# Optimization experiments

Measured on AMD Instinct MI355X. Metric: run time of the kernel, lower is better.

The kernel has to match this reference:

```python
import jax, jax.numpy as jnp
import numpy as np

N_HEAD, D_MODEL, D_K, D_V = 16, 1024, 64, 64
LN_EPS = 1e-5


def setup_inputs() -> dict:
    key = jax.random.key(0)
    ks = jax.random.split(key, 10)
    B, S = 2, 2048
    s = 1.0 / np.sqrt(D_MODEL)
    return {
        "q": jax.random.normal(ks[0], (B, S, D_MODEL), jnp.float32),
        "k": jax.random.normal(ks[1], (B, S, D_MODEL), jnp.float32),
        "v": jax.random.normal(ks[2], (B, S, D_MODEL), jnp.float32),
        "w_q": jax.random.normal(ks[3], (D_MODEL, N_HEAD * D_K), jnp.float32) * s,
        "w_k": jax.random.normal(ks[4], (D_MODEL, N_HEAD * D_K), jnp.float32) * s,
        "w_v": jax.random.normal(ks[5], (D_MODEL, N_HEAD * D_V), jnp.float32) * s,
        "w_fc": jax.random.normal(ks[6], (N_HEAD * D_V, D_MODEL), jnp.float32) * s,
        "b_fc": jnp.zeros((D_MODEL,), jnp.float32),
        "ln_g": jnp.ones((D_MODEL,), jnp.float32),
        "ln_b": jnp.zeros((D_MODEL,), jnp.float32),
    }


def _mha(q, k, v, w_q, w_k, w_v, w_fc, b_fc, ln_g, ln_b):
    B, S, _ = q.shape
    residual = q
    # projections -> [B, H, S, Dh]
    qh = (q @ w_q).reshape(B, S, N_HEAD, D_K).transpose(0, 2, 1, 3)
    kh = (k @ w_k).reshape(B, S, N_HEAD, D_K).transpose(0, 2, 1, 3)
    vh = (v @ w_v).reshape(B, S, N_HEAD, D_V).transpose(0, 2, 1, 3)
    # NOTE: original scales by sqrt(d_model), not sqrt(d_k)
    temper = jnp.sqrt(jnp.asarray(D_MODEL, qh.dtype))
    attn = jnp.einsum("bhqd,bhkd->bhqk", qh, kh) / temper
    attn = jax.nn.softmax(attn, axis=-1)  # dropout = identity (eval mode)
    out = jnp.einsum("bhqk,bhkd->bhqd", attn, vh)
    out = out.transpose(0, 2, 1, 3).reshape(B, S, N_HEAD * D_V)
    out = out @ w_fc + b_fc  # dropout = identity (eval mode)
    x = out + residual
    mu = jnp.mean(x, axis=-1, keepdims=True)
    var = jnp.var(x, axis=-1, keepdims=True)
    x = (x - mu) * jax.lax.rsqrt(var + LN_EPS) * ln_g + ln_b
    return x, attn


def reference(q, k, v, w_q, w_k, w_v, w_fc, b_fc, ln_g, ln_b):
    return _mha(q, k, v, w_q, w_k, w_v, w_fc, b_fc, ln_g, ln_b)
```

## Files before the change

kernel.cpp:

```cpp
#include <hip/hip_runtime.h>
#include <hip/hip_bf16.h>
#include <stdint.h>

typedef __attribute__((ext_vector_type(8))) short bf16x8;
typedef __attribute__((ext_vector_type(4))) float f32x4;

#define GLOAD16(gptr, lptr)                                              \
  __builtin_amdgcn_global_load_lds(                                      \
      (const __attribute__((address_space(1))) void*)(gptr),             \
      (__attribute__((address_space(3))) void*)(lptr), 16, 0, 0)

__device__ __forceinline__ uint32_t pack_bf16_2(float a, float b) {
  union { __hip_bfloat16 h; unsigned short u; } ca, cb;
  ca.h = __float2bfloat16(a); cb.h = __float2bfloat16(b);
  return (uint32_t)ca.u | ((uint32_t)cb.u << 16);
}

__global__ __launch_bounds__(256)
void prep_kernel(const float* __restrict__ q, const float* __restrict__ k,
                 const float* __restrict__ v,
                 __hip_bfloat16* __restrict__ q_bf, __hip_bfloat16* __restrict__ k_bf,
                 __hip_bfloat16* __restrict__ v_bf,
                 const float* __restrict__ w0, const float* __restrict__ w1,
                 const float* __restrict__ w2, const float* __restrict__ w3,
                 __hip_bfloat16* __restrict__ o0, __hip_bfloat16* __restrict__ o1,
                 __hip_bfloat16* __restrict__ o2, __hip_bfloat16* __restrict__ o3)
{
  const int blk = blockIdx.x;
  if (blk < 6144) {
    const int z = blk >> 11;
    const int bx = blk & 2047;
    const float* in = z == 0 ? q : z == 1 ? k : v;
    __hip_bfloat16* out = z == 0 ? q_bf : z == 1 ? k_bf : v_bf;
    long i = ((long)bx * 256 + threadIdx.x) * 8;
    float4 a = *(const float4*)(in + i);
    float4 b = *(const float4*)(in + i + 4);
    uint4 r;
    r.x = pack_bf16_2(a.x, a.y); r.y = pack_bf16_2(a.z, a.w);
    r.z = pack_bf16_2(b.x, b.y); r.w = pack_bf16_2(b.z, b.w);
    *(uint4*)(out + i) = r;
  } else {
    __shared__ float t[64][65];
    const int w = blk - 6144;
    const int z = w >> 8;
    const int by = (w >> 4) & 15, bx = w & 15;
    const float* in = z == 0 ? w0 : z == 1 ? w1 : z == 2 ? w2 : w3;
    __hip_bfloat16* out = z == 0 ? o0 : z == 1 ? o1 : z == 2 ? o2 : o3;
    const int tx = threadIdx.x & 15, ty = threadIdx.x >> 4;
    for (int i = 0; i < 4; ++i)
      for (int j = 0; j < 4; ++j)
        t[ty*4+i][tx*4+j] = in[(long)(by*64 + ty*4+i)*1024 + bx*64 + tx*4 + j];
    __syncthreads();
    for (int i = 0; i < 4; ++i)
      for (int j = 0; j < 4; ++j)
        out[(long)(bx*64 + ty*4+i)*1024 + by*64 + tx*4 + j] =
            __float2bfloat16(t[tx*4+j][ty*4+i]);
  }
}

__global__ __launch_bounds__(256)
void vtrans_kernel(const __hip_bfloat16* __restrict__ in, __hip_bfloat16* __restrict__ out)
{
  __shared__ __hip_bfloat16 t[64][72];
  const int tx = threadIdx.x & 15, ty = threadIdx.x >> 4;
  const int sb = blockIdx.x, bh = blockIdx.y;
  const __hip_bfloat16* inp = in + (long)bh * 2048 * 64;
  __hip_bfloat16* outp = out + (long)bh * 64 * 2048;
  for (int i = 0; i < 4; ++i)
    for (int j = 0; j < 4; ++j)
      t[ty*4+i][tx*4+j] = inp[(long)(sb*64 + ty*4+i)*64 + tx*4 + j];
  __syncthreads();
  for (int i = 0; i < 4; ++i)
    for (int j = 0; j < 4; ++j)
      outp[(long)(ty*4+i)*2048 + sb*64 + tx*4 + j] = t[tx*4+j][ty*4+i];
}

template<int EPI>
__global__ __launch_bounds__(256)
void gemm_bt(const __hip_bfloat16* __restrict__ A0,
             const __hip_bfloat16* __restrict__ A1,
             const __hip_bfloat16* __restrict__ A2,
             const __hip_bfloat16* __restrict__ B0,
             const __hip_bfloat16* __restrict__ B1,
             const __hip_bfloat16* __restrict__ B2,
             void* __restrict__ out,
             const float* __restrict__ bias,
             const float* __restrict__ resid,
             int M, int N, int K)
{
  const int z = (EPI == 0) ? blockIdx.z : 0;
  const __hip_bfloat16* A  = z == 0 ? A0 : z == 1 ? A1 : A2;
  const __hip_bfloat16* Bt = z == 0 ? B0 : z == 1 ? B1 : B2;
  const float scale = (EPI == 0 && z == 0) ? 0.045084219f : 1.0f;

  __shared__ __hip_bfloat16 As[128*32];
  __shared__ __hip_bfloat16 Bs[128*32];
  const int tid = threadIdx.x;
  const int wid = tid >> 6;
  const int lane = tid & 63;
  const int lr = lane & 15, lg = lane >> 4;
  const int bm = blockIdx.y, bn = blockIdx.x;
  const int wm = wid >> 1, wn = wid & 1;

  f32x4 acc[4][4] = {};

  const int srow = tid >> 2;
  const int scol = (tid & 3) * 8;
  const __hip_bfloat16* Ag = A  + (long)(bm*128 + srow)*K + scol;
  const __hip_bfloat16* Bg = Bt + (long)(bn*128 + srow)*K + scol;
  __hip_bfloat16* AsW = &As[wid*512];
  __hip_bfloat16* BsW = &Bs[wid*512];

  for (int k0 = 0; k0 < K; k0 += 32) {
    GLOAD16(Ag + k0,          AsW);
    GLOAD16(Ag + 64*K + k0,   AsW + 2048);
    GLOAD16(Bg + k0,          BsW);
    GLOAD16(Bg + 64*K + k0,   BsW + 2048);
    __syncthreads();
    bf16x8 a[4], b[4];
    for (int m = 0; m < 4; ++m)
      a[m] = *(const bf16x8*)&As[(wm*64 + m*16 + lr)*32 + lg*8];
    for (int n = 0; n < 4; ++n)
      b[n] = *(const bf16x8*)&Bs[(wn*64 + n*16 + lr)*32 + lg*8];
    for (int m = 0; m < 4; ++m)
      for (int n = 0; n < 4; ++n)
        acc[m][n] = __builtin_amdgcn_mfma_f32_16x16x32_bf16(b[n], a[m], acc[m][n], 0, 0, 0);
    __syncthreads();
  }

  for (int m = 0; m < 4; ++m) {
    const int grow = bm*128 + wm*64 + m*16 + lr;
    for (int n = 0; n < 4; ++n) {
      const int c0 = bn*128 + wn*64 + n*16 + lg*4;
      if (EPI == 0) {
        const int b_ = grow >> 11, s = grow & 2047;
        const int h = c0 >> 6, d = c0 & 63;
        uint2 pk;
        pk.x = pack_bf16_2(acc[m][n][0]*scale, acc[m][n][1]*scale);
        pk.y = pack_bf16_2(acc[m][n][2]*scale, acc[m][n][3]*scale);
        *(uint2*)((__hip_bfloat16*)out + (long)z*4194304 +
                  ((long)(b_*16 + h)*2048 + s)*64 + d) = pk;
      } else {
        float4 b4 = *(const float4*)(bias + c0);
        float4 r4 = *(const float4*)(resid + (long)grow*N + c0);
        float4 o4;
        o4.x = acc[m][n][0] + b4.x + r4.x;
        o4.y = acc[m][n][1] + b4.y + r4.y;
        o4.z = acc[m][n][2] + b4.z + r4.z;
        o4.w = acc[m][n][3] + b4.w + r4.w;
        *(float4*)((float*)out + (long)grow*N + c0) = o4;
      }
    }
  }
}

__global__ __launch_bounds__(256, 4)
void attn_kernel(const __hip_bfloat16* __restrict__ Qh,
                 const __hip_bfloat16* __restrict__ Kh,
                 const __hip_bfloat16* __restrict__ Vt,
                 float* __restrict__ attn_out,
                 __hip_bfloat16* __restrict__ O)
{
  __shared__ __hip_bfloat16 Ps[64*128];
  __shared__ float red[4][64];
  __shared__ float invl[64];

  const int tid = threadIdx.x, wid = tid >> 6, lane = tid & 63;
  const int lr = lane & 15, lg = lane >> 4;
  const int orig = (blockIdx.x & 7) * 128 + (blockIdx.x >> 3);
  const int bh = orig >> 5, qb = orig & 31;

  const __hip_bfloat16* Qlane = Qh + ((long)bh*2048 + qb*64 + lr)*64 + lg*8;
  const __hip_bfloat16* Klane = Kh + (long)bh*2048*64 + (long)(wid*32 + lr)*64 + lg*8;
  const __hip_bfloat16* Vlane = Vt + (long)bh*64*2048 + (long)(wid*16 + lr)*2048 + lg*8;

  bf16x8 aq[4][2];
  for (int mq = 0; mq < 4; ++mq)
    for (int kk = 0; kk < 2; ++kk)
      aq[mq][kk] = *(const bf16x8*)(Qlane + mq*1024 + kk*32);

  float rs[4] = {0.f, 0.f, 0.f, 0.f};
  for (int kt = 0; kt < 16; ++kt) {
    bf16x8 bk[2][2];
    for (int nk = 0; nk < 2; ++nk)
      for (int kk = 0; kk < 2; ++kk)
        bk[nk][kk] = *(const bf16x8*)(Klane + kt*8192 + nk*1024 + kk*32);
    f32x4 s2[4][2] = {};
    for (int mq = 0; mq < 4; ++mq)
      for (int nk = 0; nk < 2; ++nk)
        for (int kk = 0; kk < 2; ++kk)
          s2[mq][nk] = __builtin_amdgcn_mfma_f32_16x16x32_bf16(bk[nk][kk], aq[mq][kk], s2[mq][nk], 0, 0, 0);
    for (int mq = 0; mq < 4; ++mq)
      for (int nk = 0; nk < 2; ++nk)
        for (int jj = 0; jj < 4; ++jj)
          rs[mq] += exp2f(s2[mq][nk][jj]);
  }

  for (int mq = 0; mq < 4; ++mq) {
    float e = rs[mq];
    e += __shfl_xor(e, 16);
    e += __shfl_xor(e, 32);
    rs[mq] = e;
  }
  if (lg == 0)
    for (int mq = 0; mq < 4; ++mq)
      red[wid][mq*16 + lr] = rs[mq];
  __syncthreads();
  if (tid < 64)
    invl[tid] = 1.0f / (red[0][tid] + red[1][tid] + red[2][tid] + red[3][tid]);
  __syncthreads();

  float iv[4];
  for (int mq = 0; mq < 4; ++mq) iv[mq] = invl[mq*16 + lr];

  f32x4 acc_o[4] = {};
  float* attn_row = attn_out + ((long)bh*2048 + qb*64)*2048;

#pragma unroll 1
  for (int kt = 0; kt < 16; ++kt) {
    bf16x8 bk[2][2], vb[4];
#pragma unroll
    for (int nk = 0; nk < 2; ++nk)
      for (int kk = 0; kk < 2; ++kk)
        bk[nk][kk] = *(const bf16x8*)(Klane + kt*8192 + nk*1024 + kk*32);
#pragma unroll
    for (int k2 = 0; k2 < 4; ++k2)
      vb[k2] = *(const bf16x8*)(Vlane + kt*128 + k2*32);

    f32x4 s2[4][2] = {};
    __builtin_amdgcn_s_setprio(1);
#pragma unroll
    for (int mq = 0; mq < 4; ++mq)
      for (int nk = 0; nk < 2; ++nk)
        for (int kk = 0; kk < 2; ++kk)
          s2[mq][nk] = __builtin_amdgcn_mfma_f32_16x16x32_bf16(bk[nk][kk], aq[mq][kk], s2[mq][nk], 0, 0, 0);
    __builtin_amdgcn_s_setprio(0);

#pragma unroll
    for (int mq = 0; mq < 4; ++mq) {
      const int row = mq*16 + lr;
      for (int nk = 0; nk < 2; ++nk) {
        const int kc = wid*32 + nk*16 + lg*4;
        f32x4 p;
        p[0] = exp2f(s2[mq][nk][0]) * iv[mq];
        p[1] = exp2f(s2[mq][nk][1]) * iv[mq];
        p[2] = exp2f(s2[mq][nk][2]) * iv[mq];
        p[3] = exp2f(s2[mq][nk][3]) * iv[mq];
        __builtin_nontemporal_store(p, (f32x4*)(attn_row + (long)row*2048 + kt*128 + kc));
        uint2 pb;
        pb.x = pack_bf16_2(p[0], p[1]);
        pb.y = pack_bf16_2(p[2], p[3]);
        const int boff = (row*256 + kc*2) ^ ((row & 15) << 4);
        *(uint2*)((char*)Ps + boff) = pb;
      }
    }
    __syncthreads();

    __builtin_amdgcn_s_setprio(1);
#pragma unroll
    for (int mq = 0; mq < 4; ++mq) {
      const int row = mq*16 + lr;
      for (int k2 = 0; k2 < 4; ++k2) {
        const int boff = (row*256 + (k2*32 + lg*8)*2) ^ ((row & 15) << 4);
        bf16x8 pa = *(const bf16x8*)((char*)Ps + boff);
        acc_o[mq] = __builtin_amdgcn_mfma_f32_16x16x32_bf16(vb[k2], pa, acc_o[mq], 0, 0, 0);
      }
    }
    __builtin_amdgcn_s_setprio(0);
    __syncthreads();
  }

  const int b_ = bh >> 4, h = bh & 15;
  for (int mq = 0; mq < 4; ++mq) {
    const long grow = (long)b_*2048 + qb*64 + mq*16 + lr;
    const int col = h*64 + wid*16 + lg*4;
    uint2 pk;
    pk.x = pack_bf16_2(acc_o[mq][0], acc_o[mq][1]);
    pk.y = pack_bf16_2(acc_o[mq][2], acc_o[mq][3]);
    *(uint2*)(O + grow*1024 + col) = pk;
  }
}

__global__ __launch_bounds__(256)
void ln_kernel(const float* __restrict__ xin, const float* __restrict__ gam,
               const float* __restrict__ bet, float* __restrict__ xout)
{
  const int row = blockIdx.x;
  const int tid = threadIdx.x;
  const float* xr = xin + (long)row*1024;
  float4 v = *(const float4*)(xr + tid*4);
  float s  = v.x + v.y + v.z + v.w;
  float ss = v.x*v.x + v.y*v.y + v.z*v.z + v.w*v.w;
  for (int o = 1; o < 64; o <<= 1) {
    s  += __shfl_xor(s, o, 64);
    ss += __shfl_xor(ss, o, 64);
  }
  __shared__ float rsh[4], rssh[4];
  const int wid = tid >> 6, lane = tid & 63;
  if (lane == 0) { rsh[wid] = s; rssh[wid] = ss; }
  __syncthreads();
  s  = rsh[0] + rsh[1] + rsh[2] + rsh[3];
  ss = rssh[0] + rssh[1] + rssh[2] + rssh[3];
  const float mean = s * (1.0f/1024.0f);
  const float var  = ss * (1.0f/1024.0f) - mean*mean;
  const float rstd = rsqrtf(var + 1e-5f);
  float4 g4 = *(const float4*)(gam + tid*4);
  float4 b4 = *(const float4*)(bet + tid*4);
  float4 o4;
  o4.x = (v.x - mean)*rstd*g4.x + b4.x;
  o4.y = (v.y - mean)*rstd*g4.y + b4.y;
  o4.z = (v.z - mean)*rstd*g4.z + b4.z;
  o4.w = (v.w - mean)*rstd*g4.w + b4.w;
  *(float4*)(xout + (long)row*1024 + tid*4) = o4;
}

extern "C" void kernel_launch(void* const* d_in, const int* in_sizes, int n_in,
                              void* d_out, int out_size, void* d_ws, size_t ws_size,
                              hipStream_t stream)
{
  (void)in_sizes; (void)n_in; (void)out_size; (void)ws_size;
  const float* q    = (const float*)d_in[0];
  const float* k    = (const float*)d_in[1];
  const float* v    = (const float*)d_in[2];
  const float* w_q  = (const float*)d_in[3];
  const float* w_k  = (const float*)d_in[4];
  const float* w_v  = (const float*)d_in[5];
  const float* w_fc = (const float*)d_in[6];
  const float* b_fc = (const float*)d_in[7];
  const float* ln_g = (const float*)d_in[8];
  const float* ln_b = (const float*)d_in[9];

  const long MB = 1024*1024;
  char* ws = (char*)d_ws;
  __hip_bfloat16* q_bf  = (__hip_bfloat16*)(ws);
  __hip_bfloat16* k_bf  = (__hip_bfloat16*)(ws +  8*MB);
  __hip_bfloat16* v_bf  = (__hip_bfloat16*)(ws + 16*MB);
  __hip_bfloat16* wq_t  = (__hip_bfloat16*)(ws + 24*MB);
  __hip_bfloat16* wk_t  = (__hip_bfloat16*)(ws + 26*MB);
  __hip_bfloat16* wv_t  = (__hip_bfloat16*)(ws + 28*MB);
  __hip_bfloat16* wfc_t = (__hip_bfloat16*)(ws + 30*MB);
  __hip_bfloat16* QKVh  = (__hip_bfloat16*)(ws + 32*MB);
  __hip_bfloat16* Qh    = QKVh;
  __hip_bfloat16* Kh    = QKVh + 4194304L;
  __hip_bfloat16* Vh    = QKVh + 8388608L;
  __hip_bfloat16* Vht   = (__hip_bfloat16*)(ws + 56*MB);
  __hip_bfloat16* Obuf  = (__hip_bfloat16*)(ws + 64*MB);
  float*          xbuf  = (float*)(ws + 72*MB);

  float* x_out    = (float*)d_out;
  float* attn_out = x_out + 4194304L;

  prep_kernel<<<7168, 256, 0, stream>>>(q, k, v, q_bf, k_bf, v_bf,
                                        w_q, w_k, w_v, w_fc,
                                        wq_t, wk_t, wv_t, wfc_t);

  gemm_bt<0><<<dim3(8, 32, 3), 256, 0, stream>>>(q_bf, k_bf, v_bf,
                                                 wq_t, wk_t, wv_t,
                                                 QKVh, nullptr, nullptr, 4096, 1024, 1024);

  vtrans_kernel<<<dim3(32, 32), 256, 0, stream>>>(Vh, Vht);

  attn_kernel<<<1024, 256, 0, stream>>>(Qh, Kh, Vht, attn_out, Obuf);

  gemm_bt<2><<<dim3(8, 32), 256, 0, stream>>>(Obuf, nullptr, nullptr,
                                              wfc_t, nullptr, nullptr,
                                              xbuf, b_fc, q, 4096, 1024, 1024);

  ln_kernel<<<4096, 256, 0, stream>>>(xbuf, ln_g, ln_b, x_out);
}
```

Baseline: 310.6 us.

## Keep P in registers and split PV over keys with final LDS reduction

The attention kernel no longer passes the probability tile through shared memory with two barriers per key tile. K rows are permuted so each lane's QK^T output forms a PV operand directly in registers. Each wave now owns a slice of keys for all 64 output dims, so partial O accumulators (16 per lane) are summed across waves through a padded LDS buffer at the end. This removes per-iteration barriers and LDS traffic, but raises register pressure, drops the occupancy hint in launch bounds, and adds a final cross-wave reduction.

Measured after the change: 338.9 us. +9.1%, slower.

```diff
diff --git a/kernel.cpp b/kernel.cpp
--- a/kernel.cpp
+++ b/kernel.cpp
@@ -154,14 +154,14 @@
   }
 }
 
-__global__ __launch_bounds__(256, 4)
+__global__ __launch_bounds__(256)
 void attn_kernel(const __hip_bfloat16* __restrict__ Qh,
                  const __hip_bfloat16* __restrict__ Kh,
                  const __hip_bfloat16* __restrict__ Vt,
                  float* __restrict__ attn_out,
                  __hip_bfloat16* __restrict__ O)
 {
-  __shared__ __hip_bfloat16 Ps[64*128];
+  __shared__ float rbuf[4][16][68];
   __shared__ float red[4][64];
   __shared__ float invl[64];
 
@@ -170,11 +170,14 @@
   const int orig = (blockIdx.x & 7) * 128 + (blockIdx.x >> 3);
   const int bh = orig >> 5, qb = orig & 31;
 
+  const int krow = ((lr >> 2) << 3) + (lr & 3);
   const __hip_bfloat16* Qlane = Qh + ((long)bh*2048 + qb*64 + lr)*64 + lg*8;
-  const __hip_bfloat16* Klane = Kh + (long)bh*2048*64 + (long)(wid*32 + lr)*64 + lg*8;
-  const __hip_bfloat16* Vlane = Vt + (long)bh*64*2048 + (long)(wid*16 + lr)*2048 + lg*8;
+  const __hip_bfloat16* Klane = Kh + (long)bh*131072 + (long)(wid*32 + krow)*64 + lg*8;
+  const __hip_bfloat16* Vlane = Vt + (long)bh*131072 + (long)lr*2048 + wid*32 + lg*8;
+  float* attn_lane = attn_out + ((long)bh*2048 + qb*64 + lr)*2048 + wid*32 + lg*8;
 
   bf16x8 aq[4][2];
+#pragma unroll
   for (int mq = 0; mq < 4; ++mq)
     for (int kk = 0; kk < 2; ++kk)
       aq[mq][kk] = *(const bf16x8*)(Qlane + mq*1024 + kk*32);
@@ -182,20 +185,23 @@
   float rs[4] = {0.f, 0.f, 0.f, 0.f};
   for (int kt = 0; kt < 16; ++kt) {
     bf16x8 bk[2][2];
+#pragma unroll
     for (int nk = 0; nk < 2; ++nk)
       for (int kk = 0; kk < 2; ++kk)
-        bk[nk][kk] = *(const bf16x8*)(Klane + kt*8192 + nk*1024 + kk*32);
-    f32x4 s2[4][2] = {};
-    for (int mq = 0; mq < 4; ++mq)
-      for (int nk = 0; nk < 2; ++nk)
-        for (int kk = 0; kk < 2; ++kk)
-          s2[mq][nk] = __builtin_amdgcn_mfma_f32_16x16x32_bf16(bk[nk][kk], aq[mq][kk], s2[mq][nk], 0, 0, 0);
-    for (int mq = 0; mq < 4; ++mq)
-      for (int nk = 0; nk < 2; ++nk)
-        for (int jj = 0; jj < 4; ++jj)
-          rs[mq] += exp2f(s2[mq][nk][jj]);
-  }
-
+        bk[nk][kk] = *(const bf16x8*)(Klane + kt*8192 + nk*256 + kk*32);
+#pragma unroll
+    for (int mq = 0; mq < 4; ++mq) {
+      f32x4 s0 = {}, s1 = {};
+      for (int kk = 0; kk < 2; ++kk) {
+        s0 = __builtin_amdgcn_mfma_f32_16x16x32_bf16(bk[0][kk], aq[mq][kk], s0, 0, 0, 0);
+        s1 = __builtin_amdgcn_mfma_f32_16x16x32_bf16(bk[1][kk], aq[mq][kk], s1, 0, 0, 0);
+      }
+      for (int j = 0; j < 4; ++j)
+        rs[mq] += exp2f(s0[j]) + exp2f(s1[j]);
+    }
+  }
+
+#pragma unroll
   for (int mq = 0; mq < 4; ++mq) {
     float e = rs[mq];
     e += __shfl_xor(e, 16);
@@ -211,10 +217,10 @@
   __syncthreads();
 
   float iv[4];
+#pragma unroll
   for (int mq = 0; mq < 4; ++mq) iv[mq] = invl[mq*16 + lr];
 
-  f32x4 acc_o[4] = {};
-  float* attn_row = attn_out + ((long)bh*2048 + qb*64)*2048;
+  f32x4 acc[4][4] = {};
 
 #pragma unroll 1
   for (int kt = 0; kt < 16; ++kt) {
@@ -222,62 +228,63 @@
 #pragma unroll
     for (int nk = 0; nk < 2; ++nk)
       for (int kk = 0; kk < 2; ++kk)
-        bk[nk][kk] = *(const bf16x8*)(Klane + kt*8192 + nk*1024 + kk*32);
-#pragma unroll
-    for (int k2 = 0; k2 < 4; ++k2)
-      vb[k2] = *(const bf16x8*)(Vlane + kt*128 + k2*32);
-
-    f32x4 s2[4][2] = {};
-    __builtin_amdgcn_s_setprio(1);
-#pragma unroll
-    for (int mq = 0; mq < 4; ++mq)
-      for (int nk = 0; nk < 2; ++nk)
-        for (int kk = 0; kk < 2; ++kk)
-          s2[mq][nk] = __builtin_amdgcn_mfma_f32_16x16x32_bf16(bk[nk][kk], aq[mq][kk], s2[mq][nk], 0, 0, 0);
-    __builtin_amdgcn_s_setprio(0);
+        bk[nk][kk] = *(const bf16x8*)(Klane + kt*8192 + nk*256 + kk*32);
+#pragma unroll
+    for (int dt = 0; dt < 4; ++dt)
+      vb[dt] = *(const bf16x8*)(Vlane + dt*32768 + kt*128);
 
 #pragma unroll
     for (int mq = 0; mq < 4; ++mq) {
-      const int row = mq*16 + lr;
-      for (int nk = 0; nk < 2; ++nk) {
-        const int kc = wid*32 + nk*16 + lg*4;
-        f32x4 p;
-        p[0] = exp2f(s2[mq][nk][0]) * iv[mq];
-        p[1] = exp2f(s2[mq][nk][1]) * iv[mq];
-        p[2] = exp2f(s2[mq][nk][2]) * iv[mq];
-        p[3] = exp2f(s2[mq][nk][3]) * iv[mq];
-        __builtin_nontemporal_store(p, (f32x4*)(attn_row + (long)row*2048 + kt*128 + kc));
-        uint2 pb;
-        pb.x = pack_bf16_2(p[0], p[1]);
-        pb.y = pack_bf16_2(p[2], p[3]);
-        const int boff = (row*256 + kc*2) ^ ((row & 15) << 4);
-        *(uint2*)((char*)Ps + boff) = pb;
+      f32x4 s0 = {}, s1 = {};
+      __builtin_amdgcn_s_setprio(1);
+      for (int kk = 0; kk < 2; ++kk) {
+        s0 = __builtin_amdgcn_mfma_f32_16x16x32_bf16(bk[0][kk], aq[mq][kk], s0, 0, 0, 0);
+        s1 = __builtin_amdgcn_mfma_f32_16x16x32_bf16(bk[1][kk], aq[mq][kk], s1, 0, 0, 0);
       }
+      __builtin_amdgcn_s_setprio(0);
+
+      const float ivm = iv[mq];
+      f32x4 plo, phi;
+      plo[0] = exp2f(s0[0]) * ivm; plo[1] = exp2f(s0[1]) * ivm;
+      plo[2] = exp2f(s0[2]) * ivm; plo[3] = exp2f(s0[3]) * ivm;
+      phi[0] = exp2f(s1[0]) * ivm; phi[1] = exp2f(s1[1]) * ivm;
+      phi[2] = exp2f(s1[2]) * ivm; phi[3] = exp2f(s1[3]) * ivm;
+
+      float* dst = attn_lane + (long)(mq*16)*2048 + kt*128;
+      __builtin_nontemporal_store(plo, (f32x4*)dst);
+      __builtin_nontemporal_store(phi, (f32x4*)(dst + 4));
+
+      union { bf16x8 v; uint32_t w[4]; } pa;
+      pa.w[0] = pack_bf16_2(plo[0], plo[1]);
+      pa.w[1] = pack_bf16_2(plo[2], plo[3]);
+      pa.w[2] = pack_bf16_2(phi[0], phi[1]);
+      pa.w[3] = pack_bf16_2(phi[2], phi[3]);
+
+      __builtin_amdgcn_s_setprio(1);
+      for (int dt = 0; dt < 4; ++dt)
+        acc[mq][dt] = __builtin_amdgcn_mfma_f32_16x16x32_bf16(vb[dt], pa.v, acc[mq][dt], 0, 0, 0);
+      __builtin_amdgcn_s_setprio(0);
     }
-    __syncthreads();
-
-    __builtin_amdgcn_s_setprio(1);
-#pragma unroll
-    for (int mq = 0; mq < 4; ++mq) {
-      const int row = mq*16 + lr;
-      for (int k2 = 0; k2 < 4; ++k2) {
-        const int boff = (row*256 + (k2*32 + lg*8)*2) ^ ((row & 15) << 4);
-        bf16x8 pa = *(const bf16x8*)((char*)Ps + boff);
-        acc_o[mq] = __builtin_amdgcn_mfma_f32_16x16x32_bf16(vb[k2], pa, acc_o[mq], 0, 0, 0);
-      }
-    }
-    __builtin_amdgcn_s_setprio(0);
-    __syncthreads();
   }
 
   const int b_ = bh >> 4, h = bh & 15;
+  const int qq = tid >> 4, d0 = (tid & 15) * 4;
+#pragma unroll 1
   for (int mq = 0; mq < 4; ++mq) {
-    const long grow = (long)b_*2048 + qb*64 + mq*16 + lr;
-    const int col = h*64 + wid*16 + lg*4;
+    __syncthreads();
+#pragma unroll
+    for (int dt = 0; dt < 4; ++dt)
+      *(f32x4*)&rbuf[wid][lr][dt*16 + lg*4] = acc[mq][dt];
+    __syncthreads();
+    f32x4 a0 = *(const f32x4*)&rbuf[0][qq][d0];
+    f32x4 a1 = *(const f32x4*)&rbuf[1][qq][d0];
+    f32x4 a2 = *(const f32x4*)&rbuf[2][qq][d0];
+    f32x4 a3 = *(const f32x4*)&rbuf[3][qq][d0];
+    f32x4 s = (a0 + a1) + (a2 + a3);
     uint2 pk;
-    pk.x = pack_bf16_2(acc_o[mq][0], acc_o[mq][1]);
-    pk.y = pack_bf16_2(acc_o[mq][2], acc_o[mq][3]);
-    *(uint2*)(O + grow*1024 + col) = pk;
+    pk.x = pack_bf16_2(s[0], s[1]);
+    pk.y = pack_bf16_2(s[2], s[3]);
+    *(uint2*)(O + (long)(b_*2048 + qb*64 + mq*16 + qq)*1024 + h*64 + d0) = pk;
   }
 }
 
```
